# Optimization experiments

Measured on AMD Instinct MI355X. Metric: run time of the kernel, lower is better.

The kernel has to match this reference:

```python
import jax, jax.numpy as jnp
import numpy as np

S, B, I, H = 512, 64, 256, 512


def _uniform(key, shape, fan_in):
    bound = 1.0 / np.sqrt(fan_in)
    return jax.random.uniform(key, shape, jnp.float32, -bound, bound)


def setup_inputs() -> dict:
    key = jax.random.key(0)
    ks = jax.random.split(key, 17)
    inp = {"x": jax.random.normal(ks[0], (S, B, I), jnp.float32)}
    names = ["f", "i", "o", "g"]
    k = 1
    for n in names:
        inp[f"Wx_{n}"] = _uniform(ks[k], (I, H), I); k += 1
        inp[f"bx_{n}"] = _uniform(ks[k], (H,), I); k += 1
        inp[f"Wh_{n}"] = _uniform(ks[k], (H, H), H); k += 1
        inp[f"bh_{n}"] = _uniform(ks[k], (H,), H); k += 1
    return inp


def reference(x, Wx_f, bx_f, Wh_f, bh_f,
              Wx_i, bx_i, Wh_i, bh_i,
              Wx_o, bx_o, Wh_o, bh_o,
              Wx_g, bx_g, Wh_g, bh_g):
    # Fuse the 4 input-side and 4 hidden-side gate GEMMs into single GEMMs.
    Wx = jnp.concatenate([Wx_f, Wx_i, Wx_o, Wx_g], axis=1)   # (I, 4H)
    bx = jnp.concatenate([bx_f, bx_i, bx_o, bx_g], axis=0)   # (4H,)
    Wh = jnp.concatenate([Wh_f, Wh_i, Wh_o, Wh_g], axis=1)   # (H, 4H)
    bh = jnp.concatenate([bh_f, bh_i, bh_o, bh_g], axis=0)   # (4H,)

    hidden = Wh.shape[0]
    # Precompute input projections for all timesteps: (S, B, 4H)
    xp = jnp.einsum('sbi,ih->sbh', x, Wx) + bx

    def step(carry, xp_t):
        h, c = carry                                # (B,H), (B,H)
        gates = xp_t + h @ Wh + bh                  # (B, 4H)
        f, i_g, o, g = jnp.split(gates, 4, axis=-1)
        f = jax.nn.sigmoid(f)
        i_g = jax.nn.sigmoid(i_g)
        o = jax.nn.sigmoid(o)
        g = jnp.tanh(g)
        c = f * c + i_g * g
        h = o * jnp.tanh(c)
        return (h, c), h

    h0 = jnp.zeros((x.shape[1], hidden), x.dtype)
    c0 = jnp.zeros((x.shape[1], hidden), x.dtype)
    (h, c), h_seq = jax.lax.scan(step, (h0, c0), xp)
    # Match torch module outputs: h_seq (S,B,H), final h/c with leading layer dim.
    return h_seq, h[None], c[None]
```

## Files before the change

kernel.cpp:

```cpp
#include <hip/hip_runtime.h>


#define S_LEN 512
#define NBLK  128

typedef __attribute__((ext_vector_type(8))) __bf16 bf16x8;
typedef __attribute__((ext_vector_type(4))) float  f32x4;

#define OFF_W    ((size_t)0)
#define OFF_BIAS ((size_t)3145728)
#define OFF_X    ((size_t)4194304)
#define OFF_H    ((size_t)20971520)
#define OFF_FLG  ((size_t)21102592)

__global__ void k_conv_x(const float* __restrict__ x, __bf16* __restrict__ xb) {
  int i = blockIdx.x * 256 + threadIdx.x;
  float4 v = ((const float4*)x)[i];
  union { __bf16 b[4]; uint2 u; } p;
  p.b[0] = (__bf16)v.x; p.b[1] = (__bf16)v.y;
  p.b[2] = (__bf16)v.z; p.b[3] = (__bf16)v.w;
  ((uint2*)xb)[i] = p.u;
}

__global__ void k_conv_w(const float* __restrict__ wxf, const float* __restrict__ whf,
                         const float* __restrict__ wxi, const float* __restrict__ whi,
                         const float* __restrict__ wxo, const float* __restrict__ who,
                         const float* __restrict__ wxg, const float* __restrict__ whg,
                         __bf16* __restrict__ Wswz) {
  int tid = blockIdx.x * 256 + threadIdx.x;
  int L = tid & 63;
  int q = tid >> 6;
  int kk = q % 24;
  int q2 = q / 24;
  int g  = q2 & 3;
  int hs = q2 >> 2;
  const float* Wx = (g == 0) ? wxf : (g == 1) ? wxi : (g == 2) ? wxo : wxg;
  const float* Wh = (g == 0) ? whf : (g == 1) ? whi : (g == 2) ? who : whg;
  int col = hs * 16 + (L & 15);
  int k0  = kk * 32 + (L >> 4) * 8;
  union { __bf16 b[8]; uint4 u; } p;
#pragma unroll
  for (int j = 0; j < 8; ++j) {
    int k = k0 + j;
    float v = (k < 256) ? Wx[k * 512 + col] : Wh[(k - 256) * 512 + col];
    p.b[j] = (__bf16)v;
  }
  ((uint4*)Wswz)[tid] = p.u;
}

__global__ void k_conv_bias(const float* __restrict__ bxf, const float* __restrict__ bhf,
                            const float* __restrict__ bxi, const float* __restrict__ bhi,
                            const float* __restrict__ bxo, const float* __restrict__ bho,
                            const float* __restrict__ bxg, const float* __restrict__ bhg,
                            float* __restrict__ bc) {
  int n = blockIdx.x * 256 + threadIdx.x;
  int g = n >> 9, h = n & 511;
  const float* bx = (g == 0) ? bxf : (g == 1) ? bxi : (g == 2) ? bxo : bxg;
  const float* bh = (g == 0) ? bhf : (g == 1) ? bhi : (g == 2) ? bho : bhg;
  bc[n] = bx[h] + bh[h];
}

__device__ __forceinline__ float sigm(float x) { return 1.f / (1.f + __expf(-x)); }
__device__ __forceinline__ float tanh_f(float x) { return 1.f - 2.f / (1.f + __expf(2.f * x)); }

__device__ __forceinline__ bf16x8 load_h8(const __bf16* p) {
  union { unsigned long long q[2]; bf16x8 v; } u;
  u.q[0] = __hip_atomic_load((const unsigned long long*)p,       __ATOMIC_RELAXED, __HIP_MEMORY_SCOPE_AGENT);
  u.q[1] = __hip_atomic_load((const unsigned long long*)(p + 4), __ATOMIC_RELAXED, __HIP_MEMORY_SCOPE_AGENT);
  return u.v;
}

__global__ __launch_bounds__(128, 1) void lstm_seq(
    const __bf16* __restrict__ Wswz, const float* __restrict__ bias,
    const __bf16* __restrict__ xb, __bf16* __restrict__ hb,
    unsigned int* __restrict__ flg, float* __restrict__ out) {
  const int tid  = threadIdx.x;
  const int w    = tid >> 6;
  const int L    = tid & 63;
  const int quad = L >> 4;
  const int lc   = L & 15;
  const int mt   = blockIdx.x & 3;
  const int hs   = blockIdx.x >> 2;

  __shared__ f32x4 red[4][64];

  bf16x8 Wf[12][4];
  {
    const uint4* wp = (const uint4*)Wswz;
#pragma unroll
    for (int g = 0; g < 4; ++g)
#pragma unroll
      for (int kkl = 0; kkl < 12; ++kkl) {
        int kk = w * 12 + kkl;
        uint4 u = wp[(((size_t)(hs * 4 + g) * 24 + kk) << 6) + L];
        Wf[kkl][g] = __builtin_bit_cast(bf16x8, u);
      }
  }
  float bsv[4];
#pragma unroll
  for (int g = 0; g < 4; ++g) bsv[g] = bias[g * 512 + hs * 16 + lc];

  const int row = mt * 16 + lc;
  const __bf16* px = xb + (size_t)row * 256 + quad * 8;
  const __bf16* ph0 = hb + (size_t)row * 512 + quad * 8;
  const __bf16* ph1 = ph0 + 32768;

  const int q = L & 31;
  const unsigned int* fpoll = flg + (((size_t)mt * 32 + q) << 4);
  const bool fdep = (w == 0) ? (q < 8) : (q >= 8);
  unsigned int* fmine = flg + (((size_t)mt * 32 + hs) << 4);

  f32x4 cst = {0.f, 0.f, 0.f, 0.f};

  for (int t = 0; t < S_LEN; ++t) {
    const __bf16* rd = (t & 1) ? ph1 : ph0;
    bf16x8 Af[12];

    if (w == 0) {
#pragma unroll
      for (int kkl = 0; kkl < 8; ++kkl)
        Af[kkl] = __builtin_bit_cast(bf16x8, *(const uint4*)(px + kkl * 32));
    }

    if (t > 0) {
      const unsigned int need = (unsigned int)t;
      for (;;) {
        unsigned int f = __hip_atomic_load(fpoll, __ATOMIC_RELAXED,
                                           __HIP_MEMORY_SCOPE_AGENT);
        if (__ballot(fdep && (f < need)) == 0ull) break;
      }
    }

    if (w == 0) {
#pragma unroll
      for (int kkl = 8; kkl < 12; ++kkl)
        Af[kkl] = load_h8(rd + (kkl - 8) * 32);
    } else {
#pragma unroll
      for (int kkl = 0; kkl < 12; ++kkl)
        Af[kkl] = load_h8(rd + 128 + kkl * 32);
    }

    f32x4 acc[4] = {{0,0,0,0},{0,0,0,0},{0,0,0,0},{0,0,0,0}};
#pragma unroll
    for (int kkl = 0; kkl < 12; ++kkl)
#pragma unroll
      for (int g = 0; g < 4; ++g)
        acc[g] = __builtin_amdgcn_mfma_f32_16x16x32_bf16(Af[kkl], Wf[kkl][g], acc[g], 0, 0, 0);

    if (w == 0) {
#pragma unroll
      for (int g = 0; g < 4; ++g) red[g][L] = acc[g];
    }
    __syncthreads();

    if (w == 1) {
      __bf16* wr = hb + ((size_t)((t + 1) & 1)) * 32768;
#pragma unroll
      for (int g = 0; g < 4; ++g) acc[g] += red[g][L];
      const int col = hs * 16 + lc;

      float hv_[4], cn_[4];
#pragma unroll
      for (int r = 0; r < 4; ++r) {
        float fg = sigm(acc[0][r] + bsv[0]);
        float ig = sigm(acc[1][r] + bsv[1]);
        float og = sigm(acc[2][r] + bsv[2]);
        float gg = tanh_f(acc[3][r] + bsv[3]);
        float cn = fg * cst[r] + ig * gg;
        cst[r] = cn;
        cn_[r] = cn;
        hv_[r] = og * tanh_f(cn);
      }

#pragma unroll
      for (int r = 0; r < 4; ++r) {
        int orow = mt * 16 + quad * 4 + r;
        unsigned short hbits = __builtin_bit_cast(unsigned short, (__bf16)hv_[r]);
        __hip_atomic_store((unsigned short*)&wr[orow * 512 + col], hbits,
                           __ATOMIC_RELAXED, __HIP_MEMORY_SCOPE_AGENT);
      }
      asm volatile("s_waitcnt vmcnt(0)" ::: "memory");
      if (tid == 64)
        __hip_atomic_store(fmine, (unsigned int)(t + 1), __ATOMIC_RELAXED,
                           __HIP_MEMORY_SCOPE_AGENT);
      float* oseq = out + (size_t)t * 64 * 512;
#pragma unroll
      for (int r = 0; r < 4; ++r) {
        int orow = mt * 16 + quad * 4 + r;
        oseq[orow * 512 + col] = hv_[r];
        if (t == S_LEN - 1) {
          out[16777216 + orow * 512 + col] = hv_[r];
          out[16777216 + 32768 + orow * 512 + col] = cn_[r];
        }
      }
    }
    px += 64 * 256;
  }
}

extern "C" void kernel_launch(void* const* d_in, const int* in_sizes, int n_in,
                              void* d_out, int out_size, void* d_ws, size_t ws_size,
                              hipStream_t stream) {
  char* ws = (char*)d_ws;
  __bf16* Wswz = (__bf16*)(ws + OFF_W);
  float*  bias = (float*)(ws + OFF_BIAS);
  __bf16* xb   = (__bf16*)(ws + OFF_X);
  __bf16* hb   = (__bf16*)(ws + OFF_H);
  unsigned int* flg = (unsigned int*)(ws + OFF_FLG);

  hipMemsetAsync(ws + OFF_H, 0, 131072 + 8192, stream);

  k_conv_x<<<8192, 256, 0, stream>>>((const float*)d_in[0], xb);
  k_conv_w<<<768, 256, 0, stream>>>(
      (const float*)d_in[1],  (const float*)d_in[3],
      (const float*)d_in[5],  (const float*)d_in[7],
      (const float*)d_in[9],  (const float*)d_in[11],
      (const float*)d_in[13], (const float*)d_in[15],
      Wswz);
  k_conv_bias<<<8, 256, 0, stream>>>(
      (const float*)d_in[2],  (const float*)d_in[4],
      (const float*)d_in[6],  (const float*)d_in[8],
      (const float*)d_in[10], (const float*)d_in[12],
      (const float*)d_in[14], (const float*)d_in[16],
      bias);
  lstm_seq<<<NBLK, 128, 0, stream>>>(Wswz, bias, xb, hb, flg, (float*)d_out);
}
```

Before: 1.810 ms.

## Replace per-block flags with step-tagged hidden-state words and overlap x-projection MFMAs

Each hidden value is now stored as a 32-bit word holding the bf16 value plus the step number, so consumers poll the data itself instead of separate per-block flags. This removes the producer's s_waitcnt and flag store and the extra flag round trip on every step. Wave 0 also runs the input-projection MFMAs before waiting on the hidden state, hiding part of the barrier latency. The cost is double the hidden-state traffic, repeated polling of the full data region, and more register pressure from the 48-element q array.

```diff
diff --git a/kernel.cpp b/kernel.cpp
--- a/kernel.cpp
+++ b/kernel.cpp
@@ -11,7 +11,6 @@
 #define OFF_BIAS ((size_t)3145728)
 #define OFF_X    ((size_t)4194304)
 #define OFF_H    ((size_t)20971520)
-#define OFF_FLG  ((size_t)21102592)
 
 __global__ void k_conv_x(const float* __restrict__ x, __bf16* __restrict__ xb) {
   int i = blockIdx.x * 256 + threadIdx.x;
@@ -63,17 +62,10 @@
 __device__ __forceinline__ float sigm(float x) { return 1.f / (1.f + __expf(-x)); }
 __device__ __forceinline__ float tanh_f(float x) { return 1.f - 2.f / (1.f + __expf(2.f * x)); }
 
-__device__ __forceinline__ bf16x8 load_h8(const __bf16* p) {
-  union { unsigned long long q[2]; bf16x8 v; } u;
-  u.q[0] = __hip_atomic_load((const unsigned long long*)p,       __ATOMIC_RELAXED, __HIP_MEMORY_SCOPE_AGENT);
-  u.q[1] = __hip_atomic_load((const unsigned long long*)(p + 4), __ATOMIC_RELAXED, __HIP_MEMORY_SCOPE_AGENT);
-  return u.v;
-}
-
 __global__ __launch_bounds__(128, 1) void lstm_seq(
     const __bf16* __restrict__ Wswz, const float* __restrict__ bias,
-    const __bf16* __restrict__ xb, __bf16* __restrict__ hb,
-    unsigned int* __restrict__ flg, float* __restrict__ out) {
+    const __bf16* __restrict__ xb, unsigned int* __restrict__ hw,
+    float* __restrict__ out) {
   const int tid  = threadIdx.x;
   const int w    = tid >> 6;
   const int L    = tid & 63;
@@ -102,60 +94,97 @@
 
   const int row = mt * 16 + lc;
   const __bf16* px = xb + (size_t)row * 256 + quad * 8;
-  const __bf16* ph0 = hb + (size_t)row * 512 + quad * 8;
-  const __bf16* ph1 = ph0 + 32768;
-
-  const int q = L & 31;
-  const unsigned int* fpoll = flg + (((size_t)mt * 32 + q) << 4);
-  const bool fdep = (w == 0) ? (q < 8) : (q >= 8);
-  unsigned int* fmine = flg + (((size_t)mt * 32 + hs) << 4);
+  const unsigned int* ph0 = hw + (size_t)row * 512 + quad * 8;
+  const unsigned int* ph1 = ph0 + 32768;
 
   f32x4 cst = {0.f, 0.f, 0.f, 0.f};
 
   for (int t = 0; t < S_LEN; ++t) {
-    const __bf16* rd = (t & 1) ? ph1 : ph0;
-    bf16x8 Af[12];
+    const unsigned int* rdw = (t & 1) ? ph1 : ph0;
+    const unsigned int tagv = (unsigned int)t;
+    const unsigned long long tagpat =
+        ((unsigned long long)tagv << 16) | ((unsigned long long)tagv << 48);
+    const unsigned long long tagmask = 0xFFFF0000FFFF0000ull;
+
+    f32x4 acc[4] = {{0,0,0,0},{0,0,0,0},{0,0,0,0},{0,0,0,0}};
 
     if (w == 0) {
+      bf16x8 Ax[8];
 #pragma unroll
       for (int kkl = 0; kkl < 8; ++kkl)
-        Af[kkl] = __builtin_bit_cast(bf16x8, *(const uint4*)(px + kkl * 32));
+        Ax[kkl] = __builtin_bit_cast(bf16x8, *(const uint4*)(px + kkl * 32));
+#pragma unroll
+      for (int kkl = 0; kkl < 8; ++kkl)
+#pragma unroll
+        for (int g = 0; g < 4; ++g)
+          acc[g] = __builtin_amdgcn_mfma_f32_16x16x32_bf16(Ax[kkl], Wf[kkl][g], acc[g], 0, 0, 0);
+
+      unsigned long long q[16];
+      for (;;) {
+#pragma unroll
+        for (int f = 0; f < 4; ++f)
+#pragma unroll
+          for (int j = 0; j < 4; ++j)
+            q[f * 4 + j] = __hip_atomic_load(
+                (const unsigned long long*)(rdw + f * 32) + j,
+                __ATOMIC_RELAXED, __HIP_MEMORY_SCOPE_AGENT);
+        unsigned long long st = 0;
+#pragma unroll
+        for (int i = 0; i < 16; ++i) st |= (q[i] ^ tagpat) & tagmask;
+        if (__ballot(st != 0ull) == 0ull) break;
+      }
+#pragma unroll
+      for (int f = 0; f < 4; ++f) {
+        uint4 d;
+        unsigned long long v0 = q[f * 4 + 0], v1 = q[f * 4 + 1];
+        unsigned long long v2 = q[f * 4 + 2], v3 = q[f * 4 + 3];
+        d.x = (unsigned int)(v0 & 0xFFFFu) | (unsigned int)((v0 >> 16) & 0xFFFF0000u);
+        d.y = (unsigned int)(v1 & 0xFFFFu) | (unsigned int)((v1 >> 16) & 0xFFFF0000u);
+        d.z = (unsigned int)(v2 & 0xFFFFu) | (unsigned int)((v2 >> 16) & 0xFFFF0000u);
+        d.w = (unsigned int)(v3 & 0xFFFFu) | (unsigned int)((v3 >> 16) & 0xFFFF0000u);
+        bf16x8 Ah = __builtin_bit_cast(bf16x8, d);
+#pragma unroll
+        for (int g = 0; g < 4; ++g)
+          acc[g] = __builtin_amdgcn_mfma_f32_16x16x32_bf16(Ah, Wf[8 + f][g], acc[g], 0, 0, 0);
+      }
+
+#pragma unroll
+      for (int g = 0; g < 4; ++g) red[g][L] = acc[g];
+    } else {
+      unsigned long long q[48];
+      for (;;) {
+#pragma unroll
+        for (int f = 0; f < 12; ++f)
+#pragma unroll
+          for (int j = 0; j < 4; ++j)
+            q[f * 4 + j] = __hip_atomic_load(
+                (const unsigned long long*)(rdw + 128 + f * 32) + j,
+                __ATOMIC_RELAXED, __HIP_MEMORY_SCOPE_AGENT);
+        unsigned long long st = 0;
+#pragma unroll
+        for (int i = 0; i < 48; ++i) st |= (q[i] ^ tagpat) & tagmask;
+        if (__ballot(st != 0ull) == 0ull) break;
+      }
+#pragma unroll
+      for (int f = 0; f < 12; ++f) {
+        uint4 d;
+        unsigned long long v0 = q[f * 4 + 0], v1 = q[f * 4 + 1];
+        unsigned long long v2 = q[f * 4 + 2], v3 = q[f * 4 + 3];
+        d.x = (unsigned int)(v0 & 0xFFFFu) | (unsigned int)((v0 >> 16) & 0xFFFF0000u);
+        d.y = (unsigned int)(v1 & 0xFFFFu) | (unsigned int)((v1 >> 16) & 0xFFFF0000u);
+        d.z = (unsigned int)(v2 & 0xFFFFu) | (unsigned int)((v2 >> 16) & 0xFFFF0000u);
+        d.w = (unsigned int)(v3 & 0xFFFFu) | (unsigned int)((v3 >> 16) & 0xFFFF0000u);
+        bf16x8 Ah = __builtin_bit_cast(bf16x8, d);
+#pragma unroll
+        for (int g = 0; g < 4; ++g)
+          acc[g] = __builtin_amdgcn_mfma_f32_16x16x32_bf16(Ah, Wf[f][g], acc[g], 0, 0, 0);
+      }
     }
 
-    if (t > 0) {
-      const unsigned int need = (unsigned int)t;
-      for (;;) {
-        unsigned int f = __hip_atomic_load(fpoll, __ATOMIC_RELAXED,
-                                           __HIP_MEMORY_SCOPE_AGENT);
-        if (__ballot(fdep && (f < need)) == 0ull) break;
-      }
-    }
-
-    if (w == 0) {
-#pragma unroll
-      for (int kkl = 8; kkl < 12; ++kkl)
-        Af[kkl] = load_h8(rd + (kkl - 8) * 32);
-    } else {
-#pragma unroll
-      for (int kkl = 0; kkl < 12; ++kkl)
-        Af[kkl] = load_h8(rd + 128 + kkl * 32);
-    }
-
-    f32x4 acc[4] = {{0,0,0,0},{0,0,0,0},{0,0,0,0},{0,0,0,0}};
-#pragma unroll
-    for (int kkl = 0; kkl < 12; ++kkl)
-#pragma unroll
-      for (int g = 0; g < 4; ++g)
-        acc[g] = __builtin_amdgcn_mfma_f32_16x16x32_bf16(Af[kkl], Wf[kkl][g], acc[g], 0, 0, 0);
-
-    if (w == 0) {
-#pragma unroll
-      for (int g = 0; g < 4; ++g) red[g][L] = acc[g];
-    }
     __syncthreads();
 
     if (w == 1) {
-      __bf16* wr = hb + ((size_t)((t + 1) & 1)) * 32768;
+      unsigned int* wrw = hw + (((t + 1) & 1) ? 32768 : 0);
 #pragma unroll
       for (int g = 0; g < 4; ++g) acc[g] += red[g][L];
       const int col = hs * 16 + lc;
@@ -176,14 +205,12 @@
 #pragma unroll
       for (int r = 0; r < 4; ++r) {
         int orow = mt * 16 + quad * 4 + r;
-        unsigned short hbits = __builtin_bit_cast(unsigned short, (__bf16)hv_[r]);
-        __hip_atomic_store((unsigned short*)&wr[orow * 512 + col], hbits,
+        unsigned int hbits =
+            (unsigned int)__builtin_bit_cast(unsigned short, (__bf16)hv_[r]);
+        unsigned int word = ((unsigned int)(t + 1) << 16) | hbits;
+        __hip_atomic_store(&wrw[orow * 512 + col], word,
                            __ATOMIC_RELAXED, __HIP_MEMORY_SCOPE_AGENT);
       }
-      asm volatile("s_waitcnt vmcnt(0)" ::: "memory");
-      if (tid == 64)
-        __hip_atomic_store(fmine, (unsigned int)(t + 1), __ATOMIC_RELAXED,
-                           __HIP_MEMORY_SCOPE_AGENT);
       float* oseq = out + (size_t)t * 64 * 512;
 #pragma unroll
       for (int r = 0; r < 4; ++r) {
@@ -206,10 +233,9 @@
   __bf16* Wswz = (__bf16*)(ws + OFF_W);
   float*  bias = (float*)(ws + OFF_BIAS);
   __bf16* xb   = (__bf16*)(ws + OFF_X);
-  __bf16* hb   = (__bf16*)(ws + OFF_H);
-  unsigned int* flg = (unsigned int*)(ws + OFF_FLG);
-
-  hipMemsetAsync(ws + OFF_H, 0, 131072 + 8192, stream);
+  unsigned int* hw = (unsigned int*)(ws + OFF_H);
+
+  hipMemsetAsync(ws + OFF_H, 0, 262144, stream);
 
   k_conv_x<<<8192, 256, 0, stream>>>((const float*)d_in[0], xb);
   k_conv_w<<<768, 256, 0, stream>>>(
@@ -224,5 +250,5 @@
       (const float*)d_in[10], (const float*)d_in[12],
       (const float*)d_in[14], (const float*)d_in[16],
       bias);
-  lstm_seq<<<NBLK, 128, 0, stream>>>(Wswz, bias, xb, hb, flg, (float*)d_out);
-}
+  lstm_seq<<<NBLK, 128, 0, stream>>>(Wswz, bias, xb, hw, (float*)d_out);
+}
```

Result: slower. 2.441 ms (+34.8%).

## Pack four hidden slices per workgroup to cut cross-block flag synchronization

Applied to the files above, without the earlier changes.

The recurrent kernel moves from 128 workgroups of 2 waves to 32 workgroups of 8 waves, with each workgroup now owning four 16-column hidden slices. Each block publishes one flag per step after an extra intra-block barrier, so pollers watch 8 flags per row tile instead of 32. The goal is to shorten the per-timestep cross-CU handshake, which sits on the serial critical path. The cost is a second __syncthreads per step and fewer CUs in use. The flag is no longer preceded by an explicit vmcnt wait, so its ordering after the h stores now depends on what the barrier emits.

```diff
diff --git a/kernel.cpp b/kernel.cpp
--- a/kernel.cpp
+++ b/kernel.cpp
@@ -2,7 +2,7 @@
 
 
 #define S_LEN 512
-#define NBLK  128
+#define NBLK  32
 
 typedef __attribute__((ext_vector_type(8))) __bf16 bf16x8;
 typedef __attribute__((ext_vector_type(4))) float  f32x4;
@@ -70,19 +70,22 @@
   return u.v;
 }
 
-__global__ __launch_bounds__(128, 1) void lstm_seq(
+__global__ __launch_bounds__(512, 1) void lstm_seq(
     const __bf16* __restrict__ Wswz, const float* __restrict__ bias,
     const __bf16* __restrict__ xb, __bf16* __restrict__ hb,
     unsigned int* __restrict__ flg, float* __restrict__ out) {
   const int tid  = threadIdx.x;
-  const int w    = tid >> 6;
+  const int wv   = tid >> 6;
+  const int kh   = wv & 1;
+  const int s    = wv >> 1;
   const int L    = tid & 63;
   const int quad = L >> 4;
   const int lc   = L & 15;
   const int mt   = blockIdx.x & 3;
-  const int hs   = blockIdx.x >> 2;
-
-  __shared__ f32x4 red[4][64];
+  const int p    = blockIdx.x >> 2;
+  const int hs   = p * 4 + s;
+
+  __shared__ f32x4 red[4][4][64];
 
   bf16x8 Wf[12][4];
   {
@@ -91,7 +94,7 @@
     for (int g = 0; g < 4; ++g)
 #pragma unroll
       for (int kkl = 0; kkl < 12; ++kkl) {
-        int kk = w * 12 + kkl;
+        int kk = kh * 12 + kkl;
         uint4 u = wp[(((size_t)(hs * 4 + g) * 24 + kk) << 6) + L];
         Wf[kkl][g] = __builtin_bit_cast(bf16x8, u);
       }
@@ -105,10 +108,10 @@
   const __bf16* ph0 = hb + (size_t)row * 512 + quad * 8;
   const __bf16* ph1 = ph0 + 32768;
 
-  const int q = L & 31;
-  const unsigned int* fpoll = flg + (((size_t)mt * 32 + q) << 4);
-  const bool fdep = (w == 0) ? (q < 8) : (q >= 8);
-  unsigned int* fmine = flg + (((size_t)mt * 32 + hs) << 4);
+  const int q = L & 7;
+  const unsigned int* fpoll = flg + (((size_t)mt * 8 + q) << 4);
+  const bool fdep = (kh == 0) ? (q < 2) : (q >= 2);
+  unsigned int* fmine = flg + (((size_t)mt * 8 + p) << 4);
 
   f32x4 cst = {0.f, 0.f, 0.f, 0.f};
 
@@ -116,7 +119,7 @@
     const __bf16* rd = (t & 1) ? ph1 : ph0;
     bf16x8 Af[12];
 
-    if (w == 0) {
+    if (kh == 0) {
 #pragma unroll
       for (int kkl = 0; kkl < 8; ++kkl)
         Af[kkl] = __builtin_bit_cast(bf16x8, *(const uint4*)(px + kkl * 32));
@@ -131,7 +134,7 @@
       }
     }
 
-    if (w == 0) {
+    if (kh == 0) {
 #pragma unroll
       for (int kkl = 8; kkl < 12; ++kkl)
         Af[kkl] = load_h8(rd + (kkl - 8) * 32);
@@ -148,19 +151,19 @@
       for (int g = 0; g < 4; ++g)
         acc[g] = __builtin_amdgcn_mfma_f32_16x16x32_bf16(Af[kkl], Wf[kkl][g], acc[g], 0, 0, 0);
 
-    if (w == 0) {
-#pragma unroll
-      for (int g = 0; g < 4; ++g) red[g][L] = acc[g];
+    if (kh == 0) {
+#pragma unroll
+      for (int g = 0; g < 4; ++g) red[s][g][L] = acc[g];
     }
     __syncthreads();
 
-    if (w == 1) {
+    float hv_[4], cn_[4];
+    if (kh == 1) {
       __bf16* wr = hb + ((size_t)((t + 1) & 1)) * 32768;
 #pragma unroll
-      for (int g = 0; g < 4; ++g) acc[g] += red[g][L];
+      for (int g = 0; g < 4; ++g) acc[g] += red[s][g][L];
       const int col = hs * 16 + lc;
 
-      float hv_[4], cn_[4];
 #pragma unroll
       for (int r = 0; r < 4; ++r) {
         float fg = sigm(acc[0][r] + bsv[0]);
@@ -180,10 +183,15 @@
         __hip_atomic_store((unsigned short*)&wr[orow * 512 + col], hbits,
                            __ATOMIC_RELAXED, __HIP_MEMORY_SCOPE_AGENT);
       }
-      asm volatile("s_waitcnt vmcnt(0)" ::: "memory");
-      if (tid == 64)
-        __hip_atomic_store(fmine, (unsigned int)(t + 1), __ATOMIC_RELAXED,
-                           __HIP_MEMORY_SCOPE_AGENT);
+    }
+    __syncthreads();
+
+    if (tid == 0)
+      __hip_atomic_store(fmine, (unsigned int)(t + 1), __ATOMIC_RELAXED,
+                         __HIP_MEMORY_SCOPE_AGENT);
+
+    if (kh == 1) {
+      const int col = hs * 16 + lc;
       float* oseq = out + (size_t)t * 64 * 512;
 #pragma unroll
       for (int r = 0; r < 4; ++r) {
@@ -224,5 +232,5 @@
       (const float*)d_in[10], (const float*)d_in[12],
       (const float*)d_in[14], (const float*)d_in[16],
       bias);
-  lstm_seq<<<NBLK, 128, 0, stream>>>(Wswz, bias, xb, hb, flg, (float*)d_out);
-}
+  lstm_seq<<<NBLK, 512, 0, stream>>>(Wswz, bias, xb, hb, flg, (float*)d_out);
+}
```

After: 4.380 ms. +141.9%, slower.
